# Performance work log

Measured on AMD Instinct MI355X. Metric: run time of the kernel, lower is better.

## Reference

```python
import jax, jax.numpy as jnp
import numpy as np

N = 50000          # nodes
E = 800000         # edges
F_IN = 128         # in_channels
C = 64             # cell channels
NCELLS = 2
STEPS = 4
MULT = 4
N_EDGE_SLOTS = 14  # 2+3+4+5 mixed-op edges per cell
N_OPS = 8          # switch_on
NUM_CLASSES = 40
BN_EPS = 1e-5
GCNII_ALPHA = 0.1


def setup_inputs() -> dict:
    key = jax.random.key(0)
    ks = jax.random.split(key, 20)
    def w(k, shape, fan_in):
        return jax.random.normal(k, shape, dtype=jnp.float32) / np.float32(np.sqrt(fan_in))
    return {
        "x": jax.random.normal(ks[0], (N, F_IN), dtype=jnp.float32),
        "edge_index": jax.random.randint(ks[1], (2, E), 0, N, dtype=jnp.int32),
        "alphas": 0.001 * jax.random.normal(ks[2], (N_EDGE_SLOTS, N_OPS), dtype=jnp.float32),
        "stem_W": w(ks[3], (F_IN, 3 * C), F_IN),
        "pre_W": w(ks[4], (F_IN, C), F_IN),
        "pre0_W0": w(ks[5], (3 * C, C), 3 * C),
        "pre1_W0": w(ks[6], (3 * C, C), 3 * C),
        "pre0_W1": w(ks[7], (3 * C, C), 3 * C),
        "pre1_W1": w(ks[8], (MULT * C, C), MULT * C),
        "W_gcn": w(ks[9], (NCELLS, N_EDGE_SLOTS, C, C), C),
        "W_sage_self": w(ks[10], (NCELLS, N_EDGE_SLOTS, C, C), C),
        "W_sage_nei": w(ks[11], (NCELLS, N_EDGE_SLOTS, C, C), C),
        "W_gin": w(ks[12], (NCELLS, N_EDGE_SLOTS, C, C), C),
        "W_gc1": w(ks[13], (NCELLS, N_EDGE_SLOTS, C, C), C),
        "W_gc2": w(ks[14], (NCELLS, N_EDGE_SLOTS, C, C), C),
        "W_mlp": w(ks[15], (NCELLS, N_EDGE_SLOTS, C, C), C),
        "W_gcnii": w(ks[16], (NCELLS, N_EDGE_SLOTS, C, C), C),
        "cls_W": w(ks[17], (MULT * C + 1, NUM_CLASSES), MULT * C + 1),
        "cls_b": jnp.zeros((NUM_CLASSES,), dtype=jnp.float32),
    }


def reference(x, edge_index, alphas, stem_W, pre_W, pre0_W0, pre1_W0, pre0_W1, pre1_W1,
              W_gcn, W_sage_self, W_sage_nei, W_gin, W_gc1, W_gc2, W_mlp, W_gcnii,
              cls_W, cls_b):
    src, dst = edge_index[0], edge_index[1]
    deg = jax.ops.segment_sum(jnp.ones((E,), jnp.float32), dst, num_segments=N)
    deg = jnp.maximum(deg, 1.0)
    inv_deg = 1.0 / deg
    inv_sqrt = jax.lax.rsqrt(deg)
    edge_norm = (inv_sqrt[src] * inv_sqrt[dst])[:, None]  # [E,1] sym-normalized coeff

    def bn(h):  # batch norm over node axis, no affine (gamma=1, beta=0)
        m = jnp.mean(h, axis=0)
        v = jnp.var(h, axis=0)
        return (h - m) * jax.lax.rsqrt(v + BN_EPS)

    def mlp(xx, W, act):  # Linear(no bias) -> BN -> optional ReLU
        h = bn(xx @ W)
        return jnp.maximum(h, 0.0) if act else h

    relu = lambda t: jnp.maximum(t, 0.0)

    def mixed_op(h, wv, ci, ej, x0):
        # shared message-passing aggregations of h over edge_index
        msg = h[src]                                             # [E,C] gather
        s_sum = jax.ops.segment_sum(msg, dst, num_segments=N)    # sum agg
        s_mean = s_sum * inv_deg[:, None]                        # mean agg
        s_norm = jax.ops.segment_sum(msg * edge_norm, dst, num_segments=N)  # gcn agg
        out = wv[1] * h                                          # skip_connect (wv[0]: none)
        out = out + wv[2] * relu(s_norm @ W_gcn[ci, ej])
        out = out + wv[3] * (h @ W_sage_self[ci, ej] + s_mean @ W_sage_nei[ci, ej])
        out = out + wv[4] * relu((h + s_sum) @ W_gin[ci, ej])
        out = out + wv[5] * (h @ W_gc1[ci, ej] + s_sum @ W_gc2[ci, ej])
        out = out + wv[6] * relu(h @ W_mlp[ci, ej])
        out = out + wv[7] * relu(((1.0 - GCNII_ALPHA) * s_norm + GCNII_ALPHA * x0) @ W_gcnii[ci, ej])
        return out

    wmix = jax.nn.softmax(alphas, axis=-1)  # [14,8], identical across cells

    s0 = s1 = mlp(x, stem_W, act=False)     # stem: MLP([in, 3C], act=None)
    x0 = mlp(x, pre_W, act=True)            # preprocess: MLP([in, C], relu)
    pre_ws = [(pre0_W0, pre1_W0), (pre0_W1, pre1_W1)]
    for ci in range(NCELLS):
        p0, p1 = pre_ws[ci]
        a = mlp(s0, p0, act=True)
        b = mlp(s1, p1, act=True)
        states = [a, b]
        offset = 0
        for _ in range(STEPS):
            s = None
            for j, h in enumerate(states):
                o = mixed_op(h, wmix[offset + j], ci, offset + j, x0)
                s = o if s is None else s + o
            offset += len(states)
            states.append(s)
        out_cell = jnp.concatenate(states[-MULT:], axis=1)  # [N, 4C]
        s0, s1 = s1, out_cell

    pooled = jnp.mean(s1, axis=1, keepdims=True)            # AdaptiveAvgPool1d(1) over channels
    logits = jnp.concatenate([pooled, s1], axis=1) @ cls_W + cls_b
    return logits
```

## Files before the change

kernel.cpp:

```cpp
#include <hip/hip_runtime.h>
#include <stdint.h>

typedef unsigned short u16;
typedef __attribute__((ext_vector_type(8))) short bh8;
typedef __attribute__((ext_vector_type(4))) float f4;

__device__ __forceinline__ float b2f(u16 u){ union{unsigned u; float f;} x; x.u = ((unsigned)u)<<16; return x.f; }
__device__ __forceinline__ u16 f2b(float f){ union{float f; unsigned u;} x; x.f = f; return (u16)((x.u + 0x7fffu + ((x.u>>16)&1u))>>16); }
__device__ __forceinline__ bh8 ld8(const u16* p){ return *reinterpret_cast<const bh8*>(p); }

__global__ void k_count_deg(const int* dst, int* deg, int E){
  int i = blockIdx.x*256 + threadIdx.x;
  if (i < E) atomicAdd(&deg[dst[i]], 1);
}

__global__ __launch_bounds__(1024) void k_scan(const int* deg, int* off, int n){
  __shared__ int wsum[16];
  __shared__ int carry_s;
  int t = threadIdx.x, lane = t & 63, wv = t >> 6;
  if (t == 0) carry_s = 0;
  __syncthreads();
  for (int base = 0; base < n; base += 1024){
    int v = (base + t < n) ? deg[base + t] : 0;
    int x = v;
    #pragma unroll
    for (int o = 1; o < 64; o <<= 1){
      int u = __shfl_up(x, (unsigned)o, 64);
      if (lane >= o) x += u;
    }
    if (lane == 63) wsum[wv] = x;
    __syncthreads();
    if (wv == 0 && lane < 16){
      int s = wsum[lane];
      #pragma unroll
      for (int o = 1; o < 16; o <<= 1){
        int u = __shfl_up(s, (unsigned)o, 64);
        if (lane >= o) s += u;
      }
      wsum[lane] = s;
    }
    __syncthreads();
    int woff = (wv == 0) ? 0 : wsum[wv-1];
    int c = carry_s;
    if (base + t < n) off[base + t] = c + woff + x - v;
    __syncthreads();
    if (t == 0) carry_s = c + wsum[15];
    __syncthreads();
  }
  if (threadIdx.x == 0) off[n] = carry_s;
}

__global__ void k_invdeg(const int* deg, const int* off, int* cursor,
                         float* inv_deg, float* inv_sqrt, int n){
  int i = blockIdx.x*256 + threadIdx.x;
  if (i < n){
    cursor[i] = off[i];
    int d = deg[i]; if (d < 1) d = 1;
    float df = (float)d;
    inv_deg[i] = 1.0f/df;
    inv_sqrt[i] = rsqrtf(df);
  }
}

__global__ void k_fill_csr(const int* src, const int* dst, const float* invs,
                           int* cursor, int2* csr, int E){
  int i = blockIdx.x*256 + threadIdx.x;
  if (i < E){
    int s = src[i];
    float w = invs[s];
    int p = atomicAdd(&cursor[dst[i]], 1);
    csr[p] = make_int2(s, __float_as_int(w));
  }
}

__global__ void k_softmax(const float* alphas, float* wmix){
  int t = threadIdx.x; int r = t >> 3, o = t & 7;
  if (r < 14){
    float v = alphas[r*8+o];
    float m = v;
    #pragma unroll
    for (int d=1; d<8; d<<=1) m = fmaxf(m, __shfl_xor(m, d, 8));
    float e = expf(v - m);
    float s = e;
    #pragma unroll
    for (int d=1; d<8; d<<=1) s += __shfl_xor(s, d, 8);
    wmix[r*8+o] = e / s;
  }
}

__global__ void k_f2b(const float* a, u16* b, int n){
  int i = blockIdx.x*256 + threadIdx.x;
  if (i < n) b[i] = f2b(a[i]);
}

__global__ void k_pack2d(const float* W, u16* Bp, int K, int ncol){
  int i = blockIdx.x*256 + threadIdx.x;
  if (i < K*ncol){
    int k = i / ncol, n = i - k*ncol;
    Bp[(size_t)n*K + k] = f2b(W[i]);
  }
}

struct PackArgs { const float* W[8]; const float* wmix; u16* dst; };
__global__ void k_pack_ops7(PackArgs P){
  int i = blockIdx.x*256 + threadIdx.x;
  if (i >= 28*7*4096) return;
  int slot28 = i / (7*4096);
  int rem = i % (7*4096);
  int mat = rem >> 12;
  int e = rem & 4095;
  int k = e >> 6, n = e & 63;
  const float* wm = P.wmix + (slot28 % 14)*8;
  size_t off = (size_t)slot28*4096 + e;
  float v = 0.f;
  switch(mat){
    case 0: v = wm[2]*P.W[0][off]; break;
    case 1: v = wm[3]*P.W[1][off] + wm[5]*P.W[4][off] + ((k==n) ? wm[1] : 0.f); break;
    case 2: v = wm[3]*P.W[2][off]; break;
    case 3: v = wm[4]*P.W[3][off]; break;
    case 4: v = wm[5]*P.W[5][off]; break;
    case 5: v = wm[6]*P.W[6][off]; break;
    case 6: v = wm[7]*P.W[7][off]; break;
  }
  P.dst[(((size_t)slot28*7 + mat)<<12) + (n<<6) + k] = f2b(v);
}

__global__ void k_pack_cls(const float* W, u16* Bp){
  int i = blockIdx.x*256 + threadIdx.x;
  if (i < 48*256){
    int n = i >> 8, k = i & 255;
    float v = 0.f;
    if (n < 40) v = W[(size_t)(1+k)*40 + n] + W[n] * (1.f/256.f);
    Bp[(size_t)n*256 + k] = f2b(v);
  }
}

template<int NT>
__global__ __launch_bounds__(256) void k_gemm(const u16* A, int lda, const u16* Bp, int K,
                                              u16* Tb, int ldT, int Nn, float* S){
  __shared__ float sred[4][NT*16][2];
  int tid = threadIdx.x, wv = tid>>6, lane = tid&63, q = lane>>4, t = lane&15;
  int row0 = blockIdx.x*128 + wv*32;
  f4 acc[2][NT];
  #pragma unroll
  for (int a=0;a<2;a++)
    #pragma unroll
    for (int b=0;b<NT;b++) acc[a][b] = (f4){0.f,0.f,0.f,0.f};
  int nkb = K >> 5;
  const u16* arow0 = A + (size_t)(row0 + t)*lda + q*8;
  const u16* arow1 = arow0 + (size_t)16*lda;
  const u16* brow  = Bp + (size_t)t*K + q*8;
  for (int kb = 0; kb < nkb; ++kb){
    bh8 a0 = ld8(arow0 + kb*32);
    bh8 a1 = ld8(arow1 + kb*32);
    #pragma unroll
    for (int nt=0; nt<NT; ++nt){
      bh8 bf = ld8(brow + (size_t)nt*16*K + kb*32);
      acc[0][nt] = __builtin_amdgcn_mfma_f32_16x16x32_bf16(a0, bf, acc[0][nt], 0, 0, 0);
      acc[1][nt] = __builtin_amdgcn_mfma_f32_16x16x32_bf16(a1, bf, acc[1][nt], 0, 0, 0);
    }
  }
  #pragma unroll
  for (int nt=0;nt<NT;nt++){
    float ps = 0.f, pq = 0.f;
    #pragma unroll
    for (int rt=0;rt<2;rt++)
      #pragma unroll
      for (int r=0;r<4;r++){
        int row = row0 + rt*16 + q*4 + r;
        float v = acc[rt][nt][r];
        if (row < Nn){
          Tb[(size_t)row*ldT + nt*16 + t] = f2b(v);
          ps += v; pq += v*v;
        }
      }
    ps += __shfl_xor(ps, 16, 64); pq += __shfl_xor(pq, 16, 64);
    ps += __shfl_xor(ps, 32, 64); pq += __shfl_xor(pq, 32, 64);
    if (q == 0){ sred[wv][nt*16 + t][0] = ps; sred[wv][nt*16 + t][1] = pq; }
  }
  __syncthreads();
  if (tid < NT*16){
    float s = sred[0][tid][0] + sred[1][tid][0] + sred[2][tid][0] + sred[3][tid][0];
    float qq = sred[0][tid][1] + sred[1][tid][1] + sred[2][tid][1] + sred[3][tid][1];
    atomicAdd(&S[tid], s);
    atomicAdd(&S[256 + tid], qq);
  }
}

__global__ void k_norm(const u16* Tb, int ldT, int ncols, int Nn, const float* S,
                       u16* out, int rs_out, int relu, float invN){
  int i = blockIdx.x*256 + threadIdx.x;
  int nv = ncols >> 3;
  if (i >= Nn*nv) return;
  int r = i / nv, c8 = (i - r*nv)*8;
  bh8 tv = ld8(Tb + (size_t)r*ldT + c8);
  bh8 ov;
  #pragma unroll
  for (int u=0; u<8; ++u){
    int c = c8 + u;
    float m = S[c]*invN;
    float var = S[256+c]*invN - m*m;
    float xv = (b2f((u16)tv[u]) - m) * rsqrtf(var + 1e-5f);
    if (relu) xv = fmaxf(xv, 0.f);
    ov[u] = (short)f2b(xv);
  }
  *reinterpret_cast<bh8*>(out + (size_t)r*rs_out + c8) = ov;
}

#define ACC4(vv, ww) { \
    float c0 = __uint_as_float((vv).x << 16); \
    float c1 = __uint_as_float((vv).x & 0xffff0000u); \
    float c2 = __uint_as_float((vv).y << 16); \
    float c3 = __uint_as_float((vv).y & 0xffff0000u); \
    s0 += c0; s1 += c1; s2 += c2; s3 += c3; \
    n0 += c0*(ww); n1 += c1*(ww); n2 += c2*(ww); n3 += c3*(ww); }

template<int SHIFT>
__global__ __launch_bounds__(256) void k_aggv(const u16* h, const int* off, const int2* csr,
                                              const float* inv_sqrt, u16* out_sum, u16* out_norm, int Nn){
  int g = blockIdx.x*4 + (threadIdx.x >> 6);
  if (g >= Nn) return;
  int lane = threadIdx.x & 63;
  int sub = lane >> 4;
  int cb = (lane & 15) << 2;
  const u16* hp = h + cb;
  float s0=0.f,s1=0.f,s2=0.f,s3=0.f;
  float n0=0.f,n1=0.f,n2=0.f,n3=0.f;
  int e0 = off[g], e1 = off[g+1];
  int e = e0 + sub;
  for (; e + 4 < e1; e += 8){
    int2 cA = csr[e];
    int2 cB = csr[e+4];
    uint2 vA = *reinterpret_cast<const uint2*>(hp + (((unsigned)cA.x) << SHIFT));
    uint2 vB = *reinterpret_cast<const uint2*>(hp + (((unsigned)cB.x) << SHIFT));
    float wA = __int_as_float(cA.y), wB = __int_as_float(cB.y);
    ACC4(vA, wA)
    ACC4(vB, wB)
  }
  if (e < e1){
    int2 cA = csr[e];
    uint2 vA = *reinterpret_cast<const uint2*>(hp + (((unsigned)cA.x) << SHIFT));
    float wA = __int_as_float(cA.y);
    ACC4(vA, wA)
  }
  s0 += __shfl_xor(s0,16,64); s1 += __shfl_xor(s1,16,64);
  s2 += __shfl_xor(s2,16,64); s3 += __shfl_xor(s3,16,64);
  n0 += __shfl_xor(n0,16,64); n1 += __shfl_xor(n1,16,64);
  n2 += __shfl_xor(n2,16,64); n3 += __shfl_xor(n3,16,64);
  s0 += __shfl_xor(s0,32,64); s1 += __shfl_xor(s1,32,64);
  s2 += __shfl_xor(s2,32,64); s3 += __shfl_xor(s3,32,64);
  n0 += __shfl_xor(n0,32,64); n1 += __shfl_xor(n1,32,64);
  n2 += __shfl_xor(n2,32,64); n3 += __shfl_xor(n3,32,64);
  if (sub == 0){
    float ig = inv_sqrt[g];
    uint2 os, on;
    os.x = (uint)f2b(s0) | ((uint)f2b(s1) << 16);
    os.y = (uint)f2b(s2) | ((uint)f2b(s3) << 16);
    on.x = (uint)f2b(n0*ig) | ((uint)f2b(n1*ig) << 16);
    on.y = (uint)f2b(n2*ig) | ((uint)f2b(n3*ig) << 16);
    *reinterpret_cast<uint2*>(out_sum + (size_t)g*64 + cb) = os;
    *reinterpret_cast<uint2*>(out_norm + (size_t)g*64 + cb) = on;
  }
}

#define ACC4AB(va, vb, ww) { \
    float a0 = __uint_as_float((va).x << 16); \
    float a1 = __uint_as_float((va).x & 0xffff0000u); \
    float a2 = __uint_as_float((va).y << 16); \
    float a3 = __uint_as_float((va).y & 0xffff0000u); \
    float b0 = __uint_as_float((vb).x << 16); \
    float b1 = __uint_as_float((vb).x & 0xffff0000u); \
    float b2 = __uint_as_float((vb).y << 16); \
    float b3 = __uint_as_float((vb).y & 0xffff0000u); \
    sa0 += a0; sa1 += a1; sa2 += a2; sa3 += a3; \
    na0 += a0*(ww); na1 += a1*(ww); na2 += a2*(ww); na3 += a3*(ww); \
    sb0 += b0; sb1 += b1; sb2 += b2; sb3 += b3; \
    nb0 += b0*(ww); nb1 += b1*(ww); nb2 += b2*(ww); nb3 += b3*(ww); }

__global__ __launch_bounds__(256) void k_agg2v(const u16* ab, const int* off, const int2* csr,
                                               const float* inv_sqrt,
                                               u16* os0, u16* on0, u16* os1, u16* on1, int Nn){
  int g = blockIdx.x*4 + (threadIdx.x >> 6);
  if (g >= Nn) return;
  int lane = threadIdx.x & 63;
  int sub = lane >> 4;
  int cb = (lane & 15) << 2;
  const u16* hp = ab + cb;
  float sa0=0.f,sa1=0.f,sa2=0.f,sa3=0.f, na0=0.f,na1=0.f,na2=0.f,na3=0.f;
  float sb0=0.f,sb1=0.f,sb2=0.f,sb3=0.f, nb0=0.f,nb1=0.f,nb2=0.f,nb3=0.f;
  int e0 = off[g], e1 = off[g+1];
  int e = e0 + sub;
  for (; e + 4 < e1; e += 8){
    int2 cA = csr[e];
    int2 cB = csr[e+4];
    const u16* rpA = hp + (((unsigned)cA.x) << 7);
    const u16* rpB = hp + (((unsigned)cB.x) << 7);
    uint2 vaA = *reinterpret_cast<const uint2*>(rpA);
    uint2 vbA = *reinterpret_cast<const uint2*>(rpA + 64);
    uint2 vaB = *reinterpret_cast<const uint2*>(rpB);
    uint2 vbB = *reinterpret_cast<const uint2*>(rpB + 64);
    float wA = __int_as_float(cA.y), wB = __int_as_float(cB.y);
    ACC4AB(vaA, vbA, wA)
    ACC4AB(vaB, vbB, wB)
  }
  if (e < e1){
    int2 cA = csr[e];
    const u16* rpA = hp + (((unsigned)cA.x) << 7);
    uint2 vaA = *reinterpret_cast<const uint2*>(rpA);
    uint2 vbA = *reinterpret_cast<const uint2*>(rpA + 64);
    float wA = __int_as_float(cA.y);
    ACC4AB(vaA, vbA, wA)
  }
  #pragma unroll
  for (int m = 16; m <= 32; m <<= 1){
    sa0 += __shfl_xor(sa0,m,64); sa1 += __shfl_xor(sa1,m,64);
    sa2 += __shfl_xor(sa2,m,64); sa3 += __shfl_xor(sa3,m,64);
    na0 += __shfl_xor(na0,m,64); na1 += __shfl_xor(na1,m,64);
    na2 += __shfl_xor(na2,m,64); na3 += __shfl_xor(na3,m,64);
    sb0 += __shfl_xor(sb0,m,64); sb1 += __shfl_xor(sb1,m,64);
    sb2 += __shfl_xor(sb2,m,64); sb3 += __shfl_xor(sb3,m,64);
    nb0 += __shfl_xor(nb0,m,64); nb1 += __shfl_xor(nb1,m,64);
    nb2 += __shfl_xor(nb2,m,64); nb3 += __shfl_xor(nb3,m,64);
  }
  if (sub == 0){
    float ig = inv_sqrt[g];
    uint2 v;
    v.x = (uint)f2b(sa0) | ((uint)f2b(sa1) << 16);
    v.y = (uint)f2b(sa2) | ((uint)f2b(sa3) << 16);
    *reinterpret_cast<uint2*>(os0 + (size_t)g*64 + cb) = v;
    v.x = (uint)f2b(na0*ig) | ((uint)f2b(na1*ig) << 16);
    v.y = (uint)f2b(na2*ig) | ((uint)f2b(na3*ig) << 16);
    *reinterpret_cast<uint2*>(on0 + (size_t)g*64 + cb) = v;
    v.x = (uint)f2b(sb0) | ((uint)f2b(sb1) << 16);
    v.y = (uint)f2b(sb2) | ((uint)f2b(sb3) << 16);
    *reinterpret_cast<uint2*>(os1 + (size_t)g*64 + cb) = v;
    v.x = (uint)f2b(nb0*ig) | ((uint)f2b(nb1*ig) << 16);
    v.y = (uint)f2b(nb2*ig) | ((uint)f2b(nb3*ig) << 16);
    *reinterpret_cast<uint2*>(on1 + (size_t)g*64 + cb) = v;
  }
}

struct StepArgs {
  const u16* h[5]; const u16* asum[5]; const u16* anorm[5];
  int rs[5]; int slot[5]; int J;
  const u16* wpk; const float* inv_deg; const u16* x0;
  u16* out; int rs_out; int Nn;
};

__device__ __forceinline__ bh8 fr_scale(bh8 a, float s){
  bh8 r;
  #pragma unroll
  for (int i=0;i<8;i++) r[i] = (short)f2b(b2f((u16)a[i]) * s);
  return r;
}
__device__ __forceinline__ bh8 fr_add(bh8 a, bh8 b){
  bh8 r;
  #pragma unroll
  for (int i=0;i<8;i++) r[i] = (short)f2b(b2f((u16)a[i]) + b2f((u16)b[i]));
  return r;
}
__device__ __forceinline__ bh8 fr_comb(bh8 a, bh8 b, float wa, float wb){
  bh8 r;
  #pragma unroll
  for (int i=0;i<8;i++) r[i] = (short)f2b(wa*b2f((u16)a[i]) + wb*b2f((u16)b[i]));
  return r;
}

__device__ __forceinline__ void mm_acc(const bh8 (&af)[2][2], const u16* wlds, int mat,
                                       int t, int q, f4 (&oacc)[2][4]){
  #pragma unroll
  for (int kb=0;kb<2;kb++)
    #pragma unroll
    for (int nt=0;nt<4;nt++){
      bh8 bf = ld8(wlds + (mat<<12) + ((nt*16+t)<<6) + ((((kb<<2)|q) ^ (t&7))<<3));
      oacc[0][nt] = __builtin_amdgcn_mfma_f32_16x16x32_bf16(af[0][kb], bf, oacc[0][nt], 0, 0, 0);
      oacc[1][nt] = __builtin_amdgcn_mfma_f32_16x16x32_bf16(af[1][kb], bf, oacc[1][nt], 0, 0, 0);
    }
}

__device__ __forceinline__ void mm_relu(const bh8 (&af)[2][2], const u16* wlds, int mat,
                                        int t, int q, f4 (&oacc)[2][4]){
  f4 p[2][4];
  #pragma unroll
  for (int a=0;a<2;a++)
    #pragma unroll
    for (int b=0;b<4;b++) p[a][b] = (f4){0.f,0.f,0.f,0.f};
  #pragma unroll
  for (int kb=0;kb<2;kb++)
    #pragma unroll
    for (int nt=0;nt<4;nt++){
      bh8 bf = ld8(wlds + (mat<<12) + ((nt*16+t)<<6) + ((((kb<<2)|q) ^ (t&7))<<3));
      p[0][nt] = __builtin_amdgcn_mfma_f32_16x16x32_bf16(af[0][kb], bf, p[0][nt], 0, 0, 0);
      p[1][nt] = __builtin_amdgcn_mfma_f32_16x16x32_bf16(af[1][kb], bf, p[1][nt], 0, 0, 0);
    }
  #pragma unroll
  for (int rt=0;rt<2;rt++)
    #pragma unroll
    for (int nt=0;nt<4;nt++)
      #pragma unroll
      for (int r=0;r<4;r++)
        oacc[rt][nt][r] += fmaxf(p[rt][nt][r], 0.f);
}

__global__ __launch_bounds__(512) __attribute__((amdgpu_waves_per_eu(2,2)))
void k_step(StepArgs A){
  __shared__ u16 wlds[7*4096];
  int tid = threadIdx.x, wv = tid>>6, lane = tid&63, q = lane>>4, t = lane&15;
  int row0 = blockIdx.x*256 + wv*32;
  int rA0 = row0 + t, rA1 = row0 + 16 + t;
  int q8 = q*8;
  float idg0 = A.inv_deg[rA0];
  float idg1 = A.inv_deg[rA1];
  const u16* xp0 = A.x0 + (size_t)rA0*64;
  const u16* xp1 = A.x0 + (size_t)rA1*64;
  bh8 fx[2][2];
  fx[0][0]=ld8(xp0+q8); fx[0][1]=ld8(xp0+32+q8); fx[1][0]=ld8(xp1+q8); fx[1][1]=ld8(xp1+32+q8);

  f4 oacc[2][4];
  #pragma unroll
  for (int a=0;a<2;a++)
    #pragma unroll
    for (int b=0;b<4;b++) oacc[a][b] = (f4){0.f,0.f,0.f,0.f};

  for (int j = 0; j < A.J; ++j){
    __syncthreads();
    const u16* wg = A.wpk + ((size_t)A.slot[j]*7 << 12);
    for (int i = tid; i < 3584; i += 512){
      int mat = i >> 9, rem = i & 511, nn = rem >> 3, kc = rem & 7;
      uint4 vch = *reinterpret_cast<const uint4*>(wg + ((size_t)mat<<12) + (nn<<6) + (kc<<3));
      *reinterpret_cast<uint4*>(&wlds[(mat<<12) + (nn<<6) + ((kc ^ (nn&7))<<3)]) = vch;
    }
    __syncthreads();

    const u16* h = A.h[j]; int rs = A.rs[j];
    const u16* hp0 = h + (size_t)rA0*rs;
    const u16* hp1 = h + (size_t)rA1*rs;
    const u16* sp0 = A.asum[j] + (size_t)rA0*64;
    const u16* sp1 = A.asum[j] + (size_t)rA1*64;
    const u16* np0 = A.anorm[j] + (size_t)rA0*64;
    const u16* np1 = A.anorm[j] + (size_t)rA1*64;

    bh8 fh[2][2], fs[2][2], ax[2][2];

    fh[0][0]=ld8(hp0+q8); fh[0][1]=ld8(hp0+32+q8); fh[1][0]=ld8(hp1+q8); fh[1][1]=ld8(hp1+32+q8);
    mm_acc(fh, wlds, 1, t, q, oacc);
    mm_relu(fh, wlds, 5, t, q, oacc);
    fs[0][0]=ld8(sp0+q8); fs[0][1]=ld8(sp0+32+q8); fs[1][0]=ld8(sp1+q8); fs[1][1]=ld8(sp1+32+q8);
    mm_acc(fs, wlds, 4, t, q, oacc);
    ax[0][0]=fr_scale(fs[0][0], idg0); ax[0][1]=fr_scale(fs[0][1], idg0);
    ax[1][0]=fr_scale(fs[1][0], idg1); ax[1][1]=fr_scale(fs[1][1], idg1);
    mm_acc(ax, wlds, 2, t, q, oacc);
    ax[0][0]=fr_add(fh[0][0], fs[0][0]); ax[0][1]=fr_add(fh[0][1], fs[0][1]);
    ax[1][0]=fr_add(fh[1][0], fs[1][0]); ax[1][1]=fr_add(fh[1][1], fs[1][1]);
    mm_relu(ax, wlds, 3, t, q, oacc);
    fs[0][0]=ld8(np0+q8); fs[0][1]=ld8(np0+32+q8); fs[1][0]=ld8(np1+q8); fs[1][1]=ld8(np1+32+q8);
    mm_relu(fs, wlds, 0, t, q, oacc);
    ax[0][0]=fr_comb(fs[0][0], fx[0][0], 0.9f, 0.1f);
    ax[0][1]=fr_comb(fs[0][1], fx[0][1], 0.9f, 0.1f);
    ax[1][0]=fr_comb(fs[1][0], fx[1][0], 0.9f, 0.1f);
    ax[1][1]=fr_comb(fs[1][1], fx[1][1], 0.9f, 0.1f);
    mm_relu(ax, wlds, 6, t, q, oacc);
  }

  #pragma unroll
  for (int rt=0;rt<2;rt++)
    #pragma unroll
    for (int nt=0;nt<4;nt++)
      #pragma unroll
      for (int r=0;r<4;r++){
        int rr = row0 + rt*16 + q*4 + r;
        if (rr < A.Nn) A.out[(size_t)rr*A.rs_out + nt*16 + t] = f2b(oacc[rt][nt][r]);
      }
}

__global__ __launch_bounds__(256) void k_cls_mm(const u16* A, const u16* Bp,
                                                const float* bvec, float* out, int Nn){
  int tid = threadIdx.x, wv = tid>>6, lane = tid&63, q = lane>>4, t = lane&15;
  int row0 = blockIdx.x*128 + wv*32;
  f4 acc[2][3];
  #pragma unroll
  for (int a=0;a<2;a++)
    #pragma unroll
    for (int b=0;b<3;b++) acc[a][b] = (f4){0.f,0.f,0.f,0.f};
  const u16* arow0 = A + (size_t)(row0 + t)*256 + q*8;
  const u16* arow1 = arow0 + (size_t)16*256;
  const u16* brow  = Bp + (size_t)t*256 + q*8;
  #pragma unroll
  for (int kb = 0; kb < 8; ++kb){
    bh8 a0 = ld8(arow0 + kb*32);
    bh8 a1 = ld8(arow1 + kb*32);
    #pragma unroll
    for (int nt=0; nt<3; ++nt){
      bh8 bf = ld8(brow + (size_t)nt*16*256 + kb*32);
      acc[0][nt] = __builtin_amdgcn_mfma_f32_16x16x32_bf16(a0, bf, acc[0][nt], 0, 0, 0);
      acc[1][nt] = __builtin_amdgcn_mfma_f32_16x16x32_bf16(a1, bf, acc[1][nt], 0, 0, 0);
    }
  }
  #pragma unroll
  for (int rt=0;rt<2;rt++)
    #pragma unroll
    for (int nt=0;nt<3;nt++){
      int col = nt*16 + t;
      #pragma unroll
      for (int r=0;r<4;r++){
        int row = row0 + rt*16 + q*4 + r;
        if (row < Nn && col < 40) out[(size_t)row*40 + col] = acc[rt][nt][r] + bvec[col];
      }
    }
}

extern "C" void kernel_launch(void* const* d_in, const int* in_sizes, int n_in,
                              void* d_out, int out_size, void* d_ws, size_t ws_size,
                              hipStream_t stream){
  (void)n_in; (void)out_size; (void)ws_size;
  const float* x      = (const float*)d_in[0];
  const int*   ei     = (const int*)d_in[1];
  const float* alphas = (const float*)d_in[2];
  const float* stem_W = (const float*)d_in[3];
  const float* pre_W  = (const float*)d_in[4];
  const float* p00    = (const float*)d_in[5];
  const float* p10    = (const float*)d_in[6];
  const float* p01    = (const float*)d_in[7];
  const float* p11    = (const float*)d_in[8];
  const float* clsW = (const float*)d_in[17];
  const float* clsb = (const float*)d_in[18];

  int N = in_sizes[0] / 128;
  int E = in_sizes[1] / 2;
  const int* esrc = ei;
  const int* edst = ei + E;

  char* p = (char*)d_ws;
  auto carve = [&](size_t bytes) -> char* {
    char* r = p; p += (bytes + 255) & ~(size_t)255; return r;
  };
  int*   deg     = (int*)carve((size_t)N*4);
  int*   off     = (int*)carve((size_t)(N+1)*4);
  int*   cursor  = (int*)carve((size_t)N*4);
  int2*  csr     = (int2*)carve((size_t)E*8);
  float* inv_deg = (float*)carve((size_t)N*4);
  float* invs    = (float*)carve((size_t)N*4);
  float* wmix    = (float*)carve(14*8*4);
  float* stats   = (float*)carve(512*4);
  u16* xb      = (u16*)carve((size_t)N*128*2);
  u16* stem_pk = (u16*)carve((size_t)192*128*2);
  u16* pre_pk  = (u16*)carve((size_t)64*128*2);
  u16* p00_pk  = (u16*)carve((size_t)64*192*2);
  u16* p10_pk  = (u16*)carve((size_t)64*192*2);
  u16* p01_pk  = (u16*)carve((size_t)64*192*2);
  u16* p11_pk  = (u16*)carve((size_t)64*256*2);
  u16* cls_pk  = (u16*)carve((size_t)48*256*2);
  u16* ops_pk  = (u16*)carve((size_t)28*7*4096*2);
  u16* T       = (u16*)carve((size_t)N*192*2);
  u16* stem_o  = (u16*)carve((size_t)N*192*2);
  u16* x0b     = (u16*)carve((size_t)N*64*2);
  u16* ab      = (u16*)carve((size_t)N*128*2);
  u16* oc0     = (u16*)carve((size_t)N*256*2);
  u16* oc1     = (u16*)carve((size_t)N*256*2);
  u16* agg     = (u16*)carve((size_t)5*2*N*64*2);
  carve(131072);

  auto aggS = [&](int j){ return agg + (size_t)j*2*N*64; };
  auto aggN = [&](int j){ return agg + (size_t)j*2*N*64 + (size_t)N*64; };

  int eg = (E + 255)/256;
  int ng = (N + 255)/256;
  int gg = (N + 127)/128;
  int gg2 = (N + 255)/256;
  int ag = (N + 3)/4;
  float invN = 1.0f/(float)N;

  hipMemsetAsync(deg, 0, (size_t)N*4, stream);
  k_count_deg<<<eg,256,0,stream>>>(edst, deg, E);
  k_scan<<<1,1024,0,stream>>>(deg, off, N);
  k_invdeg<<<ng,256,0,stream>>>(deg, off, cursor, inv_deg, invs, N);
  k_fill_csr<<<eg,256,0,stream>>>(esrc, edst, invs, cursor, csr, E);
  k_softmax<<<1,128,0,stream>>>(alphas, wmix);
  k_f2b<<<(N*128+255)/256,256,0,stream>>>(x, xb, N*128);
  k_pack2d<<<(128*192+255)/256,256,0,stream>>>(stem_W, stem_pk, 128, 192);
  k_pack2d<<<(128*64+255)/256,256,0,stream>>>(pre_W, pre_pk, 128, 64);
  k_pack2d<<<(192*64+255)/256,256,0,stream>>>(p00, p00_pk, 192, 64);
  k_pack2d<<<(192*64+255)/256,256,0,stream>>>(p10, p10_pk, 192, 64);
  k_pack2d<<<(192*64+255)/256,256,0,stream>>>(p01, p01_pk, 192, 64);
  k_pack2d<<<(256*64+255)/256,256,0,stream>>>(p11, p11_pk, 256, 64);
  k_pack_cls<<<(48*256+255)/256,256,0,stream>>>(clsW, cls_pk);
  {
    PackArgs PA;
    for (int i = 0; i < 8; ++i) PA.W[i] = (const float*)d_in[9+i];
    PA.wmix = wmix; PA.dst = ops_pk;
    k_pack_ops7<<<(28*7*4096+255)/256,256,0,stream>>>(PA);
  }

  auto mlp = [&](const u16* A, int lda, const u16* Bp, int K, int ncol, u16* outb, int rs_out, int relu){
    hipMemsetAsync(stats, 0, 512*4, stream);
    if (ncol == 192)
      hipLaunchKernelGGL(HIP_KERNEL_NAME(k_gemm<12>), dim3(gg), dim3(256), 0, stream, A, lda, Bp, K, T, ncol, N, stats);
    else
      hipLaunchKernelGGL(HIP_KERNEL_NAME(k_gemm<4>), dim3(gg), dim3(256), 0, stream, A, lda, Bp, K, T, ncol, N, stats);
    k_norm<<<((N*(ncol>>3))+255)/256,256,0,stream>>>(T, ncol, ncol, N, stats, outb, rs_out, relu, invN);
  };

  mlp(xb, 128, stem_pk, 128, 192, stem_o, 192, 0);
  mlp(xb, 128, pre_pk, 128, 64, x0b, 64, 1);

  u16* ocs[2] = {oc0, oc1};
  const int slotbase[4] = {0, 2, 5, 9};
  for (int ci = 0; ci < 2; ++ci){
    const u16* s1in = (ci == 0) ? stem_o : oc0;
    int lda1 = (ci == 0) ? 192 : 256;
    int Kb   = (ci == 0) ? 192 : 256;
    const u16* pa = (ci == 0) ? p00_pk : p01_pk;
    const u16* pb = (ci == 0) ? p10_pk : p11_pk;
    mlp(stem_o, 192, pa, 192, 64, ab, 128, 1);
    mlp(s1in, lda1, pb, Kb, 64, ab + 64, 128, 1);

    u16* oc = ocs[ci];
    const u16* wpk_cell = ops_pk + (size_t)ci*14*7*4096;

    k_agg2v<<<ag,256,0,stream>>>(ab, off, csr, invs,
                                 aggS(0), aggN(0), aggS(1), aggN(1), N);

    const u16* st[5] = { ab, ab + 64, oc + 0, oc + 64, oc + 128 };
    const int strs[5] = {128, 128, 256, 256, 256};
    for (int step = 0; step < 4; ++step){
      StepArgs SA{};
      int J = step + 2;
      for (int j = 0; j < J; ++j){
        SA.h[j] = st[j]; SA.rs[j] = strs[j];
        SA.asum[j] = aggS(j); SA.anorm[j] = aggN(j);
        SA.slot[j] = slotbase[step] + j;
      }
      SA.J = J; SA.wpk = wpk_cell; SA.inv_deg = inv_deg; SA.x0 = x0b;
      SA.out = oc + (size_t)step*64; SA.rs_out = 256; SA.Nn = N;
      k_step<<<gg2,512,0,stream>>>(SA);
      if (step < 3)
        hipLaunchKernelGGL(HIP_KERNEL_NAME(k_aggv<8>), dim3(ag), dim3(256), 0, stream,
                           oc + (size_t)step*64, off, csr, invs, aggS(step+2), aggN(step+2), N);
    }
  }

  k_cls_mm<<<gg,256,0,stream>>>(oc1, cls_pk, clsb, (float*)d_out, N);
}
```

Before: 923.4 us.

## Pre-swizzle op weights at pack time and shrink step blocks to three waves

The op-weight packer now writes the XOR-swizzled LDS layout directly, so the step kernel copies weights with a plain vectorized loop instead of recomputing swizzled addresses. All activation fragments (h, sum-agg, norm-agg) are loaded before the barrier, so global loads overlap the weight staging, and one barrier per slot is dropped. Blocks shrink from 512 to 192 threads (96 rows) with the waves-per-EU pin removed, giving more blocks and more co-resident blocks per CU. In exchange, each row of nodes now pays a larger share of the 56 KB weight reload per slot, and the extra live fragments raise register pressure.

Measured after the change: 1.174 ms. +27.2%, slower.

```diff
diff --git a/kernel.cpp b/kernel.cpp
--- a/kernel.cpp
+++ b/kernel.cpp
@@ -122,7 +122,7 @@
     case 5: v = wm[6]*P.W[6][off]; break;
     case 6: v = wm[7]*P.W[7][off]; break;
   }
-  P.dst[(((size_t)slot28*7 + mat)<<12) + (n<<6) + k] = f2b(v);
+  P.dst[(((size_t)slot28*7 + mat)<<12) + (n<<6) + (((k>>3) ^ (n&7))<<3) + (k&7)] = f2b(v);
 }
 
 __global__ void k_pack_cls(const float* W, u16* Bp){
@@ -402,11 +402,11 @@
         oacc[rt][nt][r] += fmaxf(p[rt][nt][r], 0.f);
 }
 
-__global__ __launch_bounds__(512) __attribute__((amdgpu_waves_per_eu(2,2)))
+__global__ __launch_bounds__(192)
 void k_step(StepArgs A){
   __shared__ u16 wlds[7*4096];
   int tid = threadIdx.x, wv = tid>>6, lane = tid&63, q = lane>>4, t = lane&15;
-  int row0 = blockIdx.x*256 + wv*32;
+  int row0 = blockIdx.x*96 + wv*32;
   int rA0 = row0 + t, rA1 = row0 + 16 + t;
   int q8 = q*8;
   float idg0 = A.inv_deg[rA0];
@@ -422,15 +422,12 @@
     #pragma unroll
     for (int b=0;b<4;b++) oacc[a][b] = (f4){0.f,0.f,0.f,0.f};
 
+  uint4* wdst = reinterpret_cast<uint4*>(wlds);
   for (int j = 0; j < A.J; ++j){
-    __syncthreads();
+    if (j) __syncthreads();
     const u16* wg = A.wpk + ((size_t)A.slot[j]*7 << 12);
-    for (int i = tid; i < 3584; i += 512){
-      int mat = i >> 9, rem = i & 511, nn = rem >> 3, kc = rem & 7;
-      uint4 vch = *reinterpret_cast<const uint4*>(wg + ((size_t)mat<<12) + (nn<<6) + (kc<<3));
-      *reinterpret_cast<uint4*>(&wlds[(mat<<12) + (nn<<6) + ((kc ^ (nn&7))<<3)]) = vch;
-    }
-    __syncthreads();
+    const uint4* wsrc = reinterpret_cast<const uint4*>(wg);
+    for (int i = tid; i < 3584; i += 192) wdst[i] = wsrc[i];
 
     const u16* h = A.h[j]; int rs = A.rs[j];
     const u16* hp0 = h + (size_t)rA0*rs;
@@ -440,12 +437,15 @@
     const u16* np0 = A.anorm[j] + (size_t)rA0*64;
     const u16* np1 = A.anorm[j] + (size_t)rA1*64;
 
-    bh8 fh[2][2], fs[2][2], ax[2][2];
-
+    bh8 fh[2][2], fs[2][2], fn[2][2], ax[2][2];
     fh[0][0]=ld8(hp0+q8); fh[0][1]=ld8(hp0+32+q8); fh[1][0]=ld8(hp1+q8); fh[1][1]=ld8(hp1+32+q8);
+    fs[0][0]=ld8(sp0+q8); fs[0][1]=ld8(sp0+32+q8); fs[1][0]=ld8(sp1+q8); fs[1][1]=ld8(sp1+32+q8);
+    fn[0][0]=ld8(np0+q8); fn[0][1]=ld8(np0+32+q8); fn[1][0]=ld8(np1+q8); fn[1][1]=ld8(np1+32+q8);
+
+    __syncthreads();
+
     mm_acc(fh, wlds, 1, t, q, oacc);
     mm_relu(fh, wlds, 5, t, q, oacc);
-    fs[0][0]=ld8(sp0+q8); fs[0][1]=ld8(sp0+32+q8); fs[1][0]=ld8(sp1+q8); fs[1][1]=ld8(sp1+32+q8);
     mm_acc(fs, wlds, 4, t, q, oacc);
     ax[0][0]=fr_scale(fs[0][0], idg0); ax[0][1]=fr_scale(fs[0][1], idg0);
     ax[1][0]=fr_scale(fs[1][0], idg1); ax[1][1]=fr_scale(fs[1][1], idg1);
@@ -453,12 +453,11 @@
     ax[0][0]=fr_add(fh[0][0], fs[0][0]); ax[0][1]=fr_add(fh[0][1], fs[0][1]);
     ax[1][0]=fr_add(fh[1][0], fs[1][0]); ax[1][1]=fr_add(fh[1][1], fs[1][1]);
     mm_relu(ax, wlds, 3, t, q, oacc);
-    fs[0][0]=ld8(np0+q8); fs[0][1]=ld8(np0+32+q8); fs[1][0]=ld8(np1+q8); fs[1][1]=ld8(np1+32+q8);
-    mm_relu(fs, wlds, 0, t, q, oacc);
-    ax[0][0]=fr_comb(fs[0][0], fx[0][0], 0.9f, 0.1f);
-    ax[0][1]=fr_comb(fs[0][1], fx[0][1], 0.9f, 0.1f);
-    ax[1][0]=fr_comb(fs[1][0], fx[1][0], 0.9f, 0.1f);
-    ax[1][1]=fr_comb(fs[1][1], fx[1][1], 0.9f, 0.1f);
+    mm_relu(fn, wlds, 0, t, q, oacc);
+    ax[0][0]=fr_comb(fn[0][0], fx[0][0], 0.9f, 0.1f);
+    ax[0][1]=fr_comb(fn[0][1], fx[0][1], 0.9f, 0.1f);
+    ax[1][0]=fr_comb(fn[1][0], fx[1][0], 0.9f, 0.1f);
+    ax[1][1]=fr_comb(fn[1][1], fx[1][1], 0.9f, 0.1f);
     mm_relu(ax, wlds, 6, t, q, oacc);
   }
 
@@ -566,7 +565,7 @@
   int eg = (E + 255)/256;
   int ng = (N + 255)/256;
   int gg = (N + 127)/128;
-  int gg2 = (N + 255)/256;
+  int gstep = (N + 95)/96;
   int ag = (N + 3)/4;
   float invN = 1.0f/(float)N;
 
@@ -632,7 +631,7 @@
       }
       SA.J = J; SA.wpk = wpk_cell; SA.inv_deg = inv_deg; SA.x0 = x0b;
       SA.out = oc + (size_t)step*64; SA.rs_out = 256; SA.Nn = N;
-      k_step<<<gg2,512,0,stream>>>(SA);
+      k_step<<<gstep,192,0,stream>>>(SA);
       if (step < 3)
         hipLaunchKernelGGL(HIP_KERNEL_NAME(k_aggv<8>), dim3(ag), dim3(256), 0, stream,
                            oc + (size_t)step*64, off, csr, invs, aggS(step+2), aggN(step+2), N);
```
